# Optimization experiments

Measured on AMD Instinct MI355X. Metric: run time of the kernel, lower is better.

## Reference

```python
import jax, jax.numpy as jnp
import numpy as np

BALANCE_FACTOR = 10.0  # from init_kwargs


def _foreground_mask(bboxes, H, W):
    # bboxes: [B, N, 4] int (x1, y1, x2, y2), half-open raster [y1:y2, x1:x2].
    # 2D difference-array (summed-area) trick: scatter +/-1 at box corners,
    # then double cumsum; count > 0 <=> pixel covered by >= 1 box.
    B, N, _ = bboxes.shape
    x1 = jnp.clip(bboxes[..., 0], 0, W)
    y1 = jnp.clip(bboxes[..., 1], 0, H)
    x2 = jnp.clip(bboxes[..., 2], 0, W)
    y2 = jnp.clip(bboxes[..., 3], 0, H)
    b = jnp.broadcast_to(jnp.arange(B)[:, None], (B, N))
    one = jnp.ones((B, N), jnp.int32)
    diff = jnp.zeros((B, H + 1, W + 1), jnp.int32)
    diff = (diff.at[b, y1, x1].add(one)
                .at[b, y1, x2].add(-one)
                .at[b, y2, x1].add(-one)
                .at[b, y2, x2].add(one))
    cnt = jnp.cumsum(jnp.cumsum(diff, axis=1), axis=2)[:, :H, :W]
    return cnt > 0  # [B, H, W] bool


def setup_inputs() -> dict:
    key = jax.random.key(0)
    k1, k2, k3 = jax.random.split(key, 3)
    B, H, W, N = 8, 1024, 1024, 64
    loss = jax.random.uniform(k1, (B, H, W), dtype=jnp.float32)
    pred_densities = jax.random.uniform(k2, (B, H, W), dtype=jnp.float32)
    # random valid boxes: sort coordinate pairs so x1<=x2, y1<=y2
    raw = jax.random.randint(k3, (B, N, 2, 2), 0, 1024)  # [...,(x pair),(y pair)]
    xs = jnp.sort(raw[..., 0, :], axis=-1)  # [B,N,2]
    ys = jnp.sort(raw[..., 1, :], axis=-1)  # [B,N,2]
    bboxes = jnp.stack([xs[..., 0], ys[..., 0], xs[..., 1], ys[..., 1]], axis=-1).astype(jnp.int32)
    return {"loss": loss, "pred_densities": pred_densities, "bboxes": bboxes}


def reference(loss, pred_densities, bboxes):
    B, H, W = pred_densities.shape[:3]
    fg = _foreground_mask(bboxes, H, W)  # [B,H,W] bool
    # weights = fg * balance_factor + background
    weights = jnp.where(fg, jnp.float32(BALANCE_FACTOR), jnp.float32(1.0))
    out = loss * weights
    # normalize_loss with mask=None: divide by n_pixels (H*W) then by n_img (B)
    out = out / jnp.float32(H * W)
    out = out / jnp.float32(B)
    return out
```

## Files before the change

### kernel.cpp

```cpp
#include <hip/hip_runtime.h>


#define NBOX 64

__global__ __launch_bounds__(256) void density_loss_kernel(
    const float* __restrict__ loss,
    const int4*  __restrict__ bboxes,
    float*       __restrict__ out)
{
    const int row = blockIdx.x;
    const int b   = row >> 10;
    const int y   = row & 1023;
    const int t   = threadIdx.x;
    const int px0 = t << 2;

    const int4* __restrict__ box = bboxes + b * NBOX;

    unsigned int m = 0u;
    for (int i = 0; i < NBOX; ++i) {
        const int4 bx = box[i];
        if (y >= bx.y && y < bx.w) {
            const int lo = max(bx.x, px0);
            const int hi = min(bx.z, px0 + 4);
            if (lo < hi)
                m |= ((1u << (hi - lo)) - 1u) << (lo - px0);
        }
    }

    const size_t base = (size_t)row << 10;
    const float4 l = reinterpret_cast<const float4*>(loss + base)[t];
    const float C = 0x1p-23f;

    float4 o;
    o.x = (l.x * ((m & 1u) ? 10.0f : 1.0f)) * C;
    o.y = (l.y * ((m & 2u) ? 10.0f : 1.0f)) * C;
    o.z = (l.z * ((m & 4u) ? 10.0f : 1.0f)) * C;
    o.w = (l.w * ((m & 8u) ? 10.0f : 1.0f)) * C;
    reinterpret_cast<float4*>(out + base)[t] = o;
}

extern "C" void kernel_launch(void* const* d_in, const int* in_sizes, int n_in,
                              void* d_out, int out_size, void* d_ws, size_t ws_size,
                              hipStream_t stream) {
    const float* loss   = (const float*)d_in[0];
    const int4*  bboxes = (const int4*)d_in[2];
    float*       out    = (float*)d_out;

    const int n_rows = 8 * 1024;
    density_loss_kernel<<<dim3(n_rows), dim3(256), 0, stream>>>(loss, bboxes, out);
}
```

Baseline: 120.9 us.

## Precompute per-row coverage bitmasks in a separate kernel before applying weights

Splits the work into two kernels. The first builds a 32-bit coverage word per 32 pixels for each row, with boxes staged in shared memory, so each box test is evaluated once per 32 pixels instead of once per 4. The second kernel reads one mask word and streams loss to out. This cuts redundant box-scan ALU work and global box loads, at the cost of an extra launch and a small workspace write and read.

```diff
diff --git a/kernel.cpp b/kernel.cpp
--- a/kernel.cpp
+++ b/kernel.cpp
@@ -3,39 +3,62 @@
 
 #define NBOX 64
 
-__global__ __launch_bounds__(256) void density_loss_kernel(
+__global__ __launch_bounds__(256) void build_masks_kernel(
+    const int4* __restrict__ bboxes,
+    unsigned int* __restrict__ cov)
+{
+    __shared__ int4 sbox[NBOX];
+    const int t   = threadIdx.x;
+    const int bid = blockIdx.x;
+    const int b   = bid >> 7;
+
+    if (t < NBOX)
+        sbox[t] = bboxes[b * NBOX + t];
+    __syncthreads();
+
+    const int row  = (bid << 3) + (t >> 5);
+    const int y    = row & 1023;
+    const int word = t & 31;
+    const int lo_w = word << 5;
+
+    unsigned int m = 0u;
+    #pragma unroll 8
+    for (int i = 0; i < NBOX; ++i) {
+        const int4 bx = sbox[i];
+        if (y >= bx.y && y < bx.w) {
+            const int lo = max(bx.x, lo_w);
+            const int hi = min(bx.z, lo_w + 32);
+            if (lo < hi) {
+                const int len = hi - lo;
+                const unsigned int bits =
+                    (len >= 32) ? 0xFFFFFFFFu : ((1u << len) - 1u);
+                m |= bits << (lo - lo_w);
+            }
+        }
+    }
+    cov[(bid << 8) + t] = m;
+}
+
+__global__ __launch_bounds__(256) void apply_kernel(
     const float* __restrict__ loss,
-    const int4*  __restrict__ bboxes,
-    float*       __restrict__ out)
+    const unsigned int* __restrict__ cov,
+    float* __restrict__ out)
 {
     const int row = blockIdx.x;
-    const int b   = row >> 10;
-    const int y   = row & 1023;
     const int t   = threadIdx.x;
-    const int px0 = t << 2;
 
-    const int4* __restrict__ box = bboxes + b * NBOX;
-
-    unsigned int m = 0u;
-    for (int i = 0; i < NBOX; ++i) {
-        const int4 bx = box[i];
-        if (y >= bx.y && y < bx.w) {
-            const int lo = max(bx.x, px0);
-            const int hi = min(bx.z, px0 + 4);
-            if (lo < hi)
-                m |= ((1u << (hi - lo)) - 1u) << (lo - px0);
-        }
-    }
+    const unsigned int cv = cov[(row << 5) + (t >> 3)];
+    const int sh = (t & 7) << 2;
 
     const size_t base = (size_t)row << 10;
     const float4 l = reinterpret_cast<const float4*>(loss + base)[t];
     const float C = 0x1p-23f;
 
     float4 o;
-    o.x = (l.x * ((m & 1u) ? 10.0f : 1.0f)) * C;
-    o.y = (l.y * ((m & 2u) ? 10.0f : 1.0f)) * C;
-    o.z = (l.z * ((m & 4u) ? 10.0f : 1.0f)) * C;
-    o.w = (l.w * ((m & 8u) ? 10.0f : 1.0f)) * C;
+    o.x = (l.x * (((cv >> (sh + 0)) & 1u) ? 10.0f : 1.0f)) * C;
+    o.y = (l.y * (((cv >> (sh + 1)) & 1u) ? 10.0f : 1.0f)) * C;
+    o.z = (l.z * (((cv >> (sh + 2)) & 1u) ? 10.0f : 1.0f)) * C;
+    o.w = (l.w * (((cv >> (sh + 3)) & 1u) ? 10.0f : 1.0f)) * C;
     reinterpret_cast<float4*>(out + base)[t] = o;
 }
 
@@ -45,7 +68,8 @@
     const float* loss   = (const float*)d_in[0];
     const int4*  bboxes = (const int4*)d_in[2];
     float*       out    = (float*)d_out;
+    unsigned int* cov   = (unsigned int*)d_ws;
 
-    const int n_rows = 8 * 1024;
-    density_loss_kernel<<<dim3(n_rows), dim3(256), 0, stream>>>(loss, bboxes, out);
+    build_masks_kernel<<<dim3(1024), dim3(256), 0, stream>>>(bboxes, cov);
+    apply_kernel<<<dim3(8192), dim3(256), 0, stream>>>(loss, cov, out);
 }
```

After: 112.1 us. 7.3% less time.
